# Performance work log

Measured on AMD Instinct MI355X. Metric: run time of the kernel, lower is better.

## Reference

```python
import jax, jax.numpy as jnp
import numpy as np
import math

D_MODEL = 1024
N_HEADS = 16
HEAD_DIM = D_MODEL // N_HEADS


def setup_inputs() -> dict:
    key = jax.random.key(0)
    ks = jax.random.split(key, 6)
    scale = 1.0 / math.sqrt(D_MODEL)
    x = jax.random.normal(ks[0], (4, 2048, D_MODEL), dtype=jnp.float32)
    # nn.Linear weights stored as [out, in]; we keep [in, out] for x @ W
    Wq = jax.random.uniform(ks[1], (D_MODEL, D_MODEL), jnp.float32, -scale, scale)
    Wk = jax.random.uniform(ks[2], (D_MODEL, D_MODEL), jnp.float32, -scale, scale)
    Wv = jax.random.uniform(ks[3], (D_MODEL, D_MODEL), jnp.float32, -scale, scale)
    Wo = jax.random.uniform(ks[4], (D_MODEL, D_MODEL), jnp.float32, -scale, scale)
    bo = jax.random.uniform(ks[5], (D_MODEL,), jnp.float32, -scale, scale)
    return {"x": x, "Wq": Wq, "Wk": Wk, "Wv": Wv, "Wo": Wo, "bo": bo}


def reference(x, Wq, Wk, Wv, Wo, bo):
    B, S, _ = x.shape
    H, Dh = N_HEADS, HEAD_DIM
    # project and split heads -> [B, H, S, Dh]
    q = (x @ Wq).reshape(B, S, H, Dh).transpose(0, 2, 1, 3)
    k = (x @ Wk).reshape(B, S, H, Dh).transpose(0, 2, 1, 3)
    v = (x @ Wv).reshape(B, S, H, Dh).transpose(0, 2, 1, 3)
    scores = jnp.einsum('bhqd,bhkd->bhqk', q, k) / math.sqrt(Dh)
    causal = jnp.tril(jnp.ones((S, S), dtype=bool))  # True = keep
    scores = jnp.where(causal, scores, -jnp.inf)
    attn = jax.nn.softmax(scores, axis=-1)  # dropout=0.0 -> no-op
    out = jnp.einsum('bhqk,bhkd->bhqd', attn, v)
    out = out.transpose(0, 2, 1, 3).reshape(B, S, H * Dh)
    return out @ Wo + bo
```

## Files before the change

kernel.cpp:

```cpp
#include <hip/hip_runtime.h>
#include <hip/hip_bf16.h>

#define DEV __device__ __forceinline__

typedef unsigned short u16;
typedef unsigned int u32;
typedef __bf16 bf16x8 __attribute__((ext_vector_type(8)));
typedef float f32x4 __attribute__((ext_vector_type(4)));

static constexpr int S   = 2048;
static constexpr int D   = 1024;
static constexpr int H   = 16;
static constexpr int Dh  = 64;
static constexpr int B_  = 4;
static constexpr int M   = B_ * S;

DEV u16 f2bf(float f) {
    __hip_bfloat16 h = __float2bfloat16(f);
    union { __hip_bfloat16 h; u16 u; } cv; cv.h = h; return cv.u;
}
DEV float bf2f(u16 u) {
    union { u16 u; __hip_bfloat16 h; } cv; cv.u = u; return __bfloat162float(cv.h);
}
DEV f32x4 mfma16(bf16x8 a, bf16x8 b, f32x4 c) {
    return __builtin_amdgcn_mfma_f32_16x16x32_bf16(a, b, c, 0, 0, 0);
}
DEV void llds16(const u16* g, u16* l) {
    __builtin_amdgcn_global_load_lds(
        (const __attribute__((address_space(1))) u32*)g,
        (__attribute__((address_space(3))) u32*)l, 16, 0, 0);
}
DEV bf16x8 ld8f(const float* p) {
    const f32x4* q = reinterpret_cast<const f32x4*>(p);
    f32x4 a = q[0], b = q[1];
    union { u16 u[8]; bf16x8 v; } r;
    r.u[0] = f2bf(a[0]); r.u[1] = f2bf(a[1]); r.u[2] = f2bf(a[2]); r.u[3] = f2bf(a[3]);
    r.u[4] = f2bf(b[0]); r.u[5] = f2bf(b[1]); r.u[6] = f2bf(b[2]); r.u[7] = f2bf(b[3]);
    return r.v;
}

__global__ __launch_bounds__(256) void x_to_bf16(
    const float* __restrict__ x, u16* __restrict__ xb)
{
    size_t i = ((size_t)blockIdx.x * 256 + threadIdx.x) * 8;
    *reinterpret_cast<bf16x8*>(xb + i) = ld8f(x + i);
}

__global__ __launch_bounds__(256) void transpose_w(
    const float* __restrict__ Wq, const float* __restrict__ Wk,
    const float* __restrict__ Wv, const float* __restrict__ Wo,
    u16* __restrict__ WT)
{
    const float* src = blockIdx.z == 0 ? Wq : blockIdx.z == 1 ? Wk
                     : blockIdx.z == 2 ? Wv : Wo;
    u16* dst = WT + (size_t)blockIdx.z * D * D;
    __shared__ u16 T[64 * 72];
    const int k0 = blockIdx.x * 64, n0 = blockIdx.y * 64;
    const int tid = threadIdx.x;
    for (int c = tid; c < 512; c += 256) {
        int r = c >> 3, cc = (c & 7) << 3;
        *reinterpret_cast<bf16x8*>(&T[r * 72 + cc]) =
            ld8f(&src[(size_t)(k0 + r) * D + n0 + cc]);
    }
    __syncthreads();
    for (int c = tid; c < 512; c += 256) {
        int r = c >> 3, cc = (c & 7) << 3;
        u16 tmp[8];
        #pragma unroll
        for (int i = 0; i < 8; ++i) tmp[i] = T[(cc + i) * 72 + r];
        *reinterpret_cast<bf16x8*>(&dst[(size_t)(n0 + r) * D + k0 + cc]) =
            *reinterpret_cast<const bf16x8*>(tmp);
    }
}

__global__ __launch_bounds__(256) void qkv_gemm128(
    const u16* __restrict__ A, const u16* __restrict__ WT,
    u16* __restrict__ qkv, u16* __restrict__ vtb)
{
    const int bm = blockIdx.x;
    const int bn = blockIdx.y;

    __shared__ u16 SB[64 * 136];
    u16* As = SB;
    u16* Bs = SB + 4096;

    const int tid  = threadIdx.x;
    const int wave = tid >> 6, ln = tid & 63;
    const int ln15 = ln & 15, quad = ln >> 4;
    const int wm = (wave >> 1) * 64, wn = (wave & 1) * 64;

    const u16* Ab = A  + (size_t)(bm * 128) * D;
    const u16* Bb = WT + (size_t)(bn * 128) * D;

    const int c0  = wave * 128 + ln;
    const int c1  = c0 + 64;
    const int r0  = c0 >> 2, o0 = (c0 & 3) * 8;
    const int r1  = c1 >> 2, o1 = (c1 & 3) * 8;

    f32x4 acc[4][4] = {};

    for (int k0 = 0; k0 < D; k0 += 32) {
        __syncthreads();
        llds16(Ab + (size_t)r0 * D + k0 + o0, &As[(wave * 2 + 0) * 512]);
        llds16(Ab + (size_t)r1 * D + k0 + o1, &As[(wave * 2 + 1) * 512]);
        llds16(Bb + (size_t)r0 * D + k0 + o0, &Bs[(wave * 2 + 0) * 512]);
        llds16(Bb + (size_t)r1 * D + k0 + o1, &Bs[(wave * 2 + 1) * 512]);
        __syncthreads();
        bf16x8 af[4], bfr[4];
        #pragma unroll
        for (int i = 0; i < 4; ++i)
            af[i] = *reinterpret_cast<const bf16x8*>(&As[(wm + i * 16 + ln15) * 32 + quad * 8]);
        #pragma unroll
        for (int j = 0; j < 4; ++j)
            bfr[j] = *reinterpret_cast<const bf16x8*>(&Bs[(wn + j * 16 + ln15) * 32 + quad * 8]);
        #pragma unroll
        for (int i = 0; i < 4; ++i)
            #pragma unroll
            for (int j = 0; j < 4; ++j)
                acc[i][j] = mfma16(af[i], bfr[j], acc[i][j]);
    }

    const int matn = bn >> 3;
    const int t0 = bm * 128, b = t0 >> 11, s0 = t0 & (S - 1);
    __syncthreads();

    if (matn < 2) {
        u16* outp = qkv + (size_t)matn * M * D;
        #pragma unroll
        for (int h2 = 0; h2 < 2; ++h2) {
            if ((wave >> 1) == h2) {
                #pragma unroll
                for (int i = 0; i < 4; ++i)
                    #pragma unroll
                    for (int j = 0; j < 4; ++j)
                        #pragma unroll
                        for (int r = 0; r < 4; ++r)
                            SB[(i * 16 + quad * 4 + r) * 136 + wn + j * 16 + ln15] =
                                f2bf(acc[i][j][r]);
            }
            __syncthreads();
            for (int c = tid; c < 1024; c += 256) {
                int r = c >> 4, cc = (c & 15) * 8;
                int head = (bn & 7) * 2 + (cc >> 6);
                int s = s0 + h2 * 64 + r;
                *reinterpret_cast<bf16x8*>(
                    &outp[(((size_t)(b * H + head)) * S + s) * Dh + (cc & 63)]) =
                    *reinterpret_cast<const bf16x8*>(&SB[r * 136 + cc]);
            }
            __syncthreads();
        }
    } else {
        #pragma unroll
        for (int h2 = 0; h2 < 2; ++h2) {
            if ((wave & 1) == h2) {
                #pragma unroll
                for (int i = 0; i < 4; ++i)
                    #pragma unroll
                    for (int j = 0; j < 4; ++j)
                        #pragma unroll
                        for (int r = 0; r < 4; ++r) {
                            int sl = wm + i * 16 + quad * 4 + r;
                            int dh = j * 16 + ln15;
                            SB[dh * 136 + sl] = f2bf(acc[i][j][r]);
                        }
            }
            __syncthreads();
            const int bh = b * H + (bn & 7) * 2 + h2;
            u16* dst = vtb + (size_t)bh * Dh * S + s0;
            for (int c = tid; c < 1024; c += 256) {
                int r = c >> 4, cc = (c & 15) * 8;
                *reinterpret_cast<bf16x8*>(&dst[(size_t)r * S + cc]) =
                    *reinterpret_cast<const bf16x8*>(&SB[r * 136 + cc]);
            }
            __syncthreads();
        }
    }
}

__global__ __launch_bounds__(256) void attn_kernel(
    const u16* __restrict__ qbuf, const u16* __restrict__ kbuf,
    const u16* __restrict__ vt, u16* __restrict__ attno)
{
    const int i  = blockIdx.x;
    const int bh = blockIdx.y;
    const int b = bh >> 4, h = bh & 15;
    const int qt[2] = {i, 31 - i};

    __shared__ u16 Ks[2][64 * 64];
    __shared__ u16 Vs[2][64 * 64];
    __shared__ u16 Ps[4][16 * 64];

    const int tid  = threadIdx.x;
    const int wave = tid >> 6, ln = tid & 63;
    const int ln15 = ln & 15, quad = ln >> 4;
    const int swz  = ln15 & 7;

    const u16* kp0 = kbuf + (size_t)bh * S * Dh;
    const u16* vp0 = vt   + (size_t)bh * Dh * S;

    bf16x8 qf[2][2];
    #pragma unroll
    for (int t = 0; t < 2; ++t) {
        const u16* qp = qbuf + ((size_t)bh * S + qt[t] * 64) * Dh;
        for (int c = tid; c < 512; c += 256) {
            int r = c >> 3, cc = (c & 7) << 3;
            *reinterpret_cast<bf16x8*>(&Ks[0][r * 64 + cc]) =
                *reinterpret_cast<const bf16x8*>(&qp[r * 64 + cc]);
        }
        __syncthreads();
        #pragma unroll
        for (int st = 0; st < 2; ++st) {
            union { bf16x8 v; u16 u[8]; } in, ot;
            in.v = *reinterpret_cast<const bf16x8*>(&Ks[0][(wave * 16 + ln15) * 64 + st * 32 + quad * 8]);
            #pragma unroll
            for (int k = 0; k < 8; ++k) ot.u[k] = f2bf(bf2f(in.u[k]) * 0.18033688f);
            qf[t][st] = ot.v;
        }
        __syncthreads();
    }

    float l_st[2][4] = {};
    f32x4 o_st[2][4] = {};

    u16* psw = &Ps[wave][0];
    const int lrow = wave * 16 + quad * 4;

    const int c0 = wave * 128 + ln;
    const int c1 = c0 + 64;
    const int kr0 = c0 >> 3, ko0 = (((c0 & 7) ^ (kr0 & 7)) * 8);
    const int kr1 = c1 >> 3, ko1 = (((c1 & 7) ^ (kr1 & 7)) * 8);

    auto stage = [&](int kblk, int buf) {
        llds16(kp0 + ((size_t)kblk * 64 + kr0) * Dh + ko0, &Ks[buf][(wave * 2 + 0) * 512]);
        llds16(kp0 + ((size_t)kblk * 64 + kr1) * Dh + ko1, &Ks[buf][(wave * 2 + 1) * 512]);
        llds16(vp0 + (size_t)kr0 * S + kblk * 64 + ko0,    &Vs[buf][(wave * 2 + 0) * 512]);
        llds16(vp0 + (size_t)kr1 * S + kblk * 64 + ko1,    &Vs[buf][(wave * 2 + 1) * 512]);
    };

    bf16x8 kf[2][4], vf[2][4];

    auto step = [&](int t, bool domask) {
        const bf16x8* qa = qf[t];
        float* l_r = l_st[t];
        f32x4* oa = o_st[t];
        const f32x4 minit = {-24.f, -24.f, -24.f, -24.f};
        f32x4 sf[4] = {minit, minit, minit, minit};
        #pragma unroll
        for (int j = 0; j < 4; ++j) {
            sf[j] = mfma16(qa[0], kf[0][j], sf[j]);
            sf[j] = mfma16(qa[1], kf[1][j], sf[j]);
        }
        if (domask) {
            #pragma unroll
            for (int j = 0; j < 4; ++j) {
                int kg = j * 16 + ln15;
                #pragma unroll
                for (int r = 0; r < 4; ++r)
                    if (kg > lrow + r) sf[j][r] = -3e38f;
            }
        }
        #pragma unroll
        for (int j = 0; j < 4; ++j)
            #pragma unroll
            for (int r = 0; r < 4; ++r) {
                float p = exp2f(sf[j][r]);
                sf[j][r] = p;
                l_r[r] += p;
            }
        #pragma unroll
        for (int j = 0; j < 4; ++j)
            #pragma unroll
            for (int r = 0; r < 4; ++r) {
                int q = quad * 4 + r;
                int phys = ((j * 2 + (ln15 >> 3)) ^ (q & 7)) * 8 + (ln15 & 7);
                psw[q * 64 + phys] = f2bf(sf[j][r]);
            }

        #pragma unroll
        for (int st = 0; st < 2; ++st) {
            bf16x8 pa = *reinterpret_cast<const bf16x8*>(
                &psw[ln15 * 64 + ((st * 4 + quad) ^ swz) * 8]);
            #pragma unroll
            for (int jd = 0; jd < 4; ++jd)
                oa[jd] = mfma16(pa, vf[st][jd], oa[jd]);
        }
    };

    const int nstage = qt[1] + 1;
    stage(0, 0);
    int cur = 0;
    for (int kblk = 0; kblk < nstage; ++kblk) {
        __syncthreads();
        if (kblk + 1 < nstage) stage(kblk + 1, cur ^ 1);
        #pragma unroll
        for (int st = 0; st < 2; ++st)
            #pragma unroll
            for (int j = 0; j < 4; ++j) {
                kf[st][j] = *reinterpret_cast<const bf16x8*>(
                    &Ks[cur][(j * 16 + ln15) * 64 + ((st * 4 + quad) ^ swz) * 8]);
                vf[st][j] = *reinterpret_cast<const bf16x8*>(
                    &Vs[cur][(j * 16 + ln15) * 64 + ((st * 4 + quad) ^ swz) * 8]);
            }
        step(1, kblk == qt[1]);
        if (kblk <= qt[0]) step(0, kblk == qt[0]);
        cur ^= 1;
    }

    #pragma unroll
    for (int t = 0; t < 2; ++t) {
        float linv[4];
        #pragma unroll
        for (int r = 0; r < 4; ++r) {
            float l = l_st[t][r];
            l += __shfl_xor(l, 1, 64);
            l += __shfl_xor(l, 2, 64);
            l += __shfl_xor(l, 4, 64);
            l += __shfl_xor(l, 8, 64);
            linv[r] = 1.0f / l;
        }
        #pragma unroll
        for (int jd = 0; jd < 4; ++jd)
            #pragma unroll
            for (int r = 0; r < 4; ++r) {
                int qrow = qt[t] * 64 + wave * 16 + quad * 4 + r;
                size_t off = ((size_t)(b * S + qrow)) * D + h * Dh + jd * 16 + ln15;
                attno[off] = f2bf(o_st[t][jd][r] * linv[r]);
            }
    }
}

__global__ __launch_bounds__(256) void proj_gemm128(
    const u16* __restrict__ A, const u16* __restrict__ WoT,
    const float* __restrict__ bo, float* __restrict__ out)
{
    const int bm = blockIdx.x;
    const int bn = blockIdx.y;

    __shared__ u16 As[128 * 32];
    __shared__ u16 Bs[128 * 32];

    const int tid  = threadIdx.x;
    const int wave = tid >> 6, ln = tid & 63;
    const int ln15 = ln & 15, quad = ln >> 4;
    const int wm = (wave >> 1) * 64, wn = (wave & 1) * 64;

    const u16* Ab = A   + (size_t)(bm * 128) * D;
    const u16* Bb = WoT + (size_t)(bn * 128) * D;

    const int c0 = wave * 128 + ln;
    const int c1 = c0 + 64;
    const int r0 = c0 >> 2, o0 = (c0 & 3) * 8;
    const int r1 = c1 >> 2, o1 = (c1 & 3) * 8;

    f32x4 acc[4][4] = {};

    for (int k0 = 0; k0 < D; k0 += 32) {
        __syncthreads();
        llds16(Ab + (size_t)r0 * D + k0 + o0, &As[(wave * 2 + 0) * 512]);
        llds16(Ab + (size_t)r1 * D + k0 + o1, &As[(wave * 2 + 1) * 512]);
        llds16(Bb + (size_t)r0 * D + k0 + o0, &Bs[(wave * 2 + 0) * 512]);
        llds16(Bb + (size_t)r1 * D + k0 + o1, &Bs[(wave * 2 + 1) * 512]);
        __syncthreads();
        bf16x8 af[4], bfr[4];
        #pragma unroll
        for (int i = 0; i < 4; ++i)
            af[i] = *reinterpret_cast<const bf16x8*>(&As[(wm + i * 16 + ln15) * 32 + quad * 8]);
        #pragma unroll
        for (int j = 0; j < 4; ++j)
            bfr[j] = *reinterpret_cast<const bf16x8*>(&Bs[(wn + j * 16 + ln15) * 32 + quad * 8]);
        #pragma unroll
        for (int i = 0; i < 4; ++i)
            #pragma unroll
            for (int j = 0; j < 4; ++j)
                acc[i][j] = mfma16(af[i], bfr[j], acc[i][j]);
    }

    #pragma unroll
    for (int i = 0; i < 4; ++i)
        #pragma unroll
        for (int j = 0; j < 4; ++j)
            #pragma unroll
            for (int r = 0; r < 4; ++r) {
                int t   = bm * 128 + wm + i * 16 + quad * 4 + r;
                int col = bn * 128 + wn + j * 16 + ln15;
                out[(size_t)t * D + col] = acc[i][j][r] + bo[col];
            }
}

extern "C" void kernel_launch(void* const* d_in, const int* in_sizes, int n_in,
                              void* d_out, int out_size, void* d_ws, size_t ws_size,
                              hipStream_t stream) {
    const float* x  = (const float*)d_in[0];
    const float* Wq = (const float*)d_in[1];
    const float* Wk = (const float*)d_in[2];
    const float* Wv = (const float*)d_in[3];
    const float* Wo = (const float*)d_in[4];
    const float* bo = (const float*)d_in[5];
    float* out = (float*)d_out;
    u16* ws  = (u16*)d_ws;

    u16* WT   = ws;
    u16* xb   = WT + (size_t)4 * D * D;
    u16* qkvb = xb + (size_t)M * D;
    u16* kb   = qkvb + (size_t)M * D;
    u16* vtb  = qkvb + (size_t)2 * M * D;
    u16* attn = xb;

    x_to_bf16   <<<dim3(M * D / (256 * 8)), 256, 0, stream>>>(x, xb);
    transpose_w <<<dim3(16, 16, 4), 256, 0, stream>>>(Wq, Wk, Wv, Wo, WT);
    qkv_gemm128 <<<dim3(64, 24),    256, 0, stream>>>(xb, WT, qkvb, vtb);
    attn_kernel <<<dim3(16, 64),    256, 0, stream>>>(qkvb, kb, vtb, attn);
    proj_gemm128<<<dim3(64, 8),     256, 0, stream>>>(attn, WT + (size_t)3 * D * D, bo, out);
}
```

Measured before the change: 288.4 us.

## Double GEMM K-tile with swizzled LDS and give attention blocks four query tiles

Both projection GEMMs now stage 64-wide K slices into XOR-swizzled shared memory. This halves the number of barrier pairs per K loop and is meant to avoid LDS bank conflicts on fragment reads. The attention kernel now assigns four causally balanced query tiles to each block and halves the grid, so every loaded K/V tile is reused across more query tiles. The trade-off is more registers for four sets of accumulators and only 512 attention blocks, which risks lower occupancy and less parallelism.

```diff
diff --git a/kernel.cpp b/kernel.cpp
--- a/kernel.cpp
+++ b/kernel.cpp
@@ -80,44 +80,54 @@
     const int bm = blockIdx.x;
     const int bn = blockIdx.y;
 
-    __shared__ u16 SB[64 * 136];
+    __shared__ u16 SB[16384];
     u16* As = SB;
-    u16* Bs = SB + 4096;
+    u16* Bs = SB + 8192;
 
     const int tid  = threadIdx.x;
     const int wave = tid >> 6, ln = tid & 63;
     const int ln15 = ln & 15, quad = ln >> 4;
+    const int swz  = ln15 & 7;
     const int wm = (wave >> 1) * 64, wn = (wave & 1) * 64;
 
     const u16* Ab = A  + (size_t)(bm * 128) * D;
     const u16* Bb = WT + (size_t)(bn * 128) * D;
 
-    const int c0  = wave * 128 + ln;
-    const int c1  = c0 + 64;
-    const int r0  = c0 >> 2, o0 = (c0 & 3) * 8;
-    const int r1  = c1 >> 2, o1 = (c1 & 3) * 8;
+    int srow[4], soff[4];
+    #pragma unroll
+    for (int k = 0; k < 4; ++k) {
+        int ch = wave * 256 + k * 64 + ln;
+        srow[k] = ch >> 3;
+        soff[k] = ((ch & 7) ^ (srow[k] & 7)) * 8;
+    }
 
     f32x4 acc[4][4] = {};
 
-    for (int k0 = 0; k0 < D; k0 += 32) {
-        __syncthreads();
-        llds16(Ab + (size_t)r0 * D + k0 + o0, &As[(wave * 2 + 0) * 512]);
-        llds16(Ab + (size_t)r1 * D + k0 + o1, &As[(wave * 2 + 1) * 512]);
-        llds16(Bb + (size_t)r0 * D + k0 + o0, &Bs[(wave * 2 + 0) * 512]);
-        llds16(Bb + (size_t)r1 * D + k0 + o1, &Bs[(wave * 2 + 1) * 512]);
-        __syncthreads();
-        bf16x8 af[4], bfr[4];
-        #pragma unroll
-        for (int i = 0; i < 4; ++i)
-            af[i] = *reinterpret_cast<const bf16x8*>(&As[(wm + i * 16 + ln15) * 32 + quad * 8]);
-        #pragma unroll
-        for (int j = 0; j < 4; ++j)
-            bfr[j] = *reinterpret_cast<const bf16x8*>(&Bs[(wn + j * 16 + ln15) * 32 + quad * 8]);
-        #pragma unroll
-        for (int i = 0; i < 4; ++i)
+    for (int k0 = 0; k0 < D; k0 += 64) {
+        __syncthreads();
+        #pragma unroll
+        for (int k = 0; k < 4; ++k) {
+            llds16(Ab + (size_t)srow[k] * D + k0 + soff[k], &As[(wave * 4 + k) * 512]);
+            llds16(Bb + (size_t)srow[k] * D + k0 + soff[k], &Bs[(wave * 4 + k) * 512]);
+        }
+        __syncthreads();
+        #pragma unroll
+        for (int ks = 0; ks < 2; ++ks) {
+            bf16x8 af[4], bfr[4];
+            #pragma unroll
+            for (int i = 0; i < 4; ++i)
+                af[i] = *reinterpret_cast<const bf16x8*>(
+                    &As[(wm + i * 16 + ln15) * 64 + ((ks * 4 + quad) ^ swz) * 8]);
             #pragma unroll
             for (int j = 0; j < 4; ++j)
-                acc[i][j] = mfma16(af[i], bfr[j], acc[i][j]);
+                bfr[j] = *reinterpret_cast<const bf16x8*>(
+                    &Bs[(wn + j * 16 + ln15) * 64 + ((ks * 4 + quad) ^ swz) * 8]);
+            #pragma unroll
+            for (int i = 0; i < 4; ++i)
+                #pragma unroll
+                for (int j = 0; j < 4; ++j)
+                    acc[i][j] = mfma16(af[i], bfr[j], acc[i][j]);
+        }
     }
 
     const int matn = bn >> 3;
@@ -184,7 +194,7 @@
     const int i  = blockIdx.x;
     const int bh = blockIdx.y;
     const int b = bh >> 4, h = bh & 15;
-    const int qt[2] = {i, 31 - i};
+    const int qt[4] = {i, 15 - i, 16 + i, 31 - i};
 
     __shared__ u16 Ks[2][64 * 64];
     __shared__ u16 Vs[2][64 * 64];
@@ -198,9 +208,9 @@
     const u16* kp0 = kbuf + (size_t)bh * S * Dh;
     const u16* vp0 = vt   + (size_t)bh * Dh * S;
 
-    bf16x8 qf[2][2];
+    bf16x8 qf[4][2];
     #pragma unroll
-    for (int t = 0; t < 2; ++t) {
+    for (int t = 0; t < 4; ++t) {
         const u16* qp = qbuf + ((size_t)bh * S + qt[t] * 64) * Dh;
         for (int c = tid; c < 512; c += 256) {
             int r = c >> 3, cc = (c & 7) << 3;
@@ -219,8 +229,8 @@
         __syncthreads();
     }
 
-    float l_st[2][4] = {};
-    f32x4 o_st[2][4] = {};
+    float l_st[4][4] = {};
+    f32x4 o_st[4][4] = {};
 
     u16* psw = &Ps[wave][0];
     const int lrow = wave * 16 + quad * 4;
@@ -286,7 +296,7 @@
         }
     };
 
-    const int nstage = qt[1] + 1;
+    const int nstage = qt[3] + 1;
     stage(0, 0);
     int cur = 0;
     for (int kblk = 0; kblk < nstage; ++kblk) {
@@ -301,13 +311,15 @@
                 vf[st][j] = *reinterpret_cast<const bf16x8*>(
                     &Vs[cur][(j * 16 + ln15) * 64 + ((st * 4 + quad) ^ swz) * 8]);
             }
-        step(1, kblk == qt[1]);
+        step(3, kblk == qt[3]);
+        if (kblk <= qt[2]) step(2, kblk == qt[2]);
+        if (kblk <= qt[1]) step(1, kblk == qt[1]);
         if (kblk <= qt[0]) step(0, kblk == qt[0]);
         cur ^= 1;
     }
 
     #pragma unroll
-    for (int t = 0; t < 2; ++t) {
+    for (int t = 0; t < 4; ++t) {
         float linv[4];
         #pragma unroll
         for (int r = 0; r < 4; ++r) {
@@ -336,43 +348,53 @@
     const int bm = blockIdx.x;
     const int bn = blockIdx.y;
 
-    __shared__ u16 As[128 * 32];
-    __shared__ u16 Bs[128 * 32];
+    __shared__ u16 As[8192];
+    __shared__ u16 Bs[8192];
 
     const int tid  = threadIdx.x;
     const int wave = tid >> 6, ln = tid & 63;
     const int ln15 = ln & 15, quad = ln >> 4;
+    const int swz  = ln15 & 7;
     const int wm = (wave >> 1) * 64, wn = (wave & 1) * 64;
 
     const u16* Ab = A   + (size_t)(bm * 128) * D;
     const u16* Bb = WoT + (size_t)(bn * 128) * D;
 
-    const int c0 = wave * 128 + ln;
-    const int c1 = c0 + 64;
-    const int r0 = c0 >> 2, o0 = (c0 & 3) * 8;
-    const int r1 = c1 >> 2, o1 = (c1 & 3) * 8;
+    int srow[4], soff[4];
+    #pragma unroll
+    for (int k = 0; k < 4; ++k) {
+        int ch = wave * 256 + k * 64 + ln;
+        srow[k] = ch >> 3;
+        soff[k] = ((ch & 7) ^ (srow[k] & 7)) * 8;
+    }
 
     f32x4 acc[4][4] = {};
 
-    for (int k0 = 0; k0 < D; k0 += 32) {
-        __syncthreads();
-        llds16(Ab + (size_t)r0 * D + k0 + o0, &As[(wave * 2 + 0) * 512]);
-        llds16(Ab + (size_t)r1 * D + k0 + o1, &As[(wave * 2 + 1) * 512]);
-        llds16(Bb + (size_t)r0 * D + k0 + o0, &Bs[(wave * 2 + 0) * 512]);
-        llds16(Bb + (size_t)r1 * D + k0 + o1, &Bs[(wave * 2 + 1) * 512]);
-        __syncthreads();
-        bf16x8 af[4], bfr[4];
-        #pragma unroll
-        for (int i = 0; i < 4; ++i)
-            af[i] = *reinterpret_cast<const bf16x8*>(&As[(wm + i * 16 + ln15) * 32 + quad * 8]);
-        #pragma unroll
-        for (int j = 0; j < 4; ++j)
-            bfr[j] = *reinterpret_cast<const bf16x8*>(&Bs[(wn + j * 16 + ln15) * 32 + quad * 8]);
-        #pragma unroll
-        for (int i = 0; i < 4; ++i)
+    for (int k0 = 0; k0 < D; k0 += 64) {
+        __syncthreads();
+        #pragma unroll
+        for (int k = 0; k < 4; ++k) {
+            llds16(Ab + (size_t)srow[k] * D + k0 + soff[k], &As[(wave * 4 + k) * 512]);
+            llds16(Bb + (size_t)srow[k] * D + k0 + soff[k], &Bs[(wave * 4 + k) * 512]);
+        }
+        __syncthreads();
+        #pragma unroll
+        for (int ks = 0; ks < 2; ++ks) {
+            bf16x8 af[4], bfr[4];
+            #pragma unroll
+            for (int i = 0; i < 4; ++i)
+                af[i] = *reinterpret_cast<const bf16x8*>(
+                    &As[(wm + i * 16 + ln15) * 64 + ((ks * 4 + quad) ^ swz) * 8]);
             #pragma unroll
             for (int j = 0; j < 4; ++j)
-                acc[i][j] = mfma16(af[i], bfr[j], acc[i][j]);
+                bfr[j] = *reinterpret_cast<const bf16x8*>(
+                    &Bs[(wn + j * 16 + ln15) * 64 + ((ks * 4 + quad) ^ swz) * 8]);
+            #pragma unroll
+            for (int i = 0; i < 4; ++i)
+                #pragma unroll
+                for (int j = 0; j < 4; ++j)
+                    acc[i][j] = mfma16(af[i], bfr[j], acc[i][j]);
+        }
     }
 
     #pragma unroll
@@ -409,6 +431,6 @@
     x_to_bf16   <<<dim3(M * D / (256 * 8)), 256, 0, stream>>>(x, xb);
     transpose_w <<<dim3(16, 16, 4), 256, 0, stream>>>(Wq, Wk, Wv, Wo, WT);
     qkv_gemm128 <<<dim3(64, 24),    256, 0, stream>>>(xb, WT, qkvb, vtb);
-    attn_kernel <<<dim3(16, 64),    256, 0, stream>>>(qkvb, kb, vtb, attn);
+    attn_kernel <<<dim3(8, 64),     256, 0, stream>>>(qkvb, kb, vtb, attn);
     proj_gemm128<<<dim3(64, 8),     256, 0, stream>>>(attn, WT + (size_t)3 * D * D, bo, out);
 }
```

After: 309.5 us. 7.3% more time.
